# Kernel tuning notes

Hardware: AMD Instinct MI355X
Metric: run time of the kernel (lower is better)

## Reference

```python
import jax, jax.numpy as jnp
import numpy as np

T = 40           # rollout steps
ATT_TEMP = 5.0   # Arbiter attention temperature
ACT_CLIP = 3.5


def setup_inputs() -> dict:
    key = jax.random.key(0)
    ks = jax.random.split(key, 6)
    B, D = 262144, 128
    # states: vel >= 0, dx > 0 (dx is a divisor)
    unscaled_s = jax.random.uniform(ks[0], (B, T, 7), dtype=jnp.float32)
    unscaled_s = unscaled_s.at[:, :, 0].set(unscaled_s[:, :, 0] * 20.0 + 5.0)   # vel
    unscaled_s = unscaled_s.at[:, :, 2].set(unscaled_s[:, :, 2] * 4.0 - 2.0)    # dv (leader)
    unscaled_s = unscaled_s.at[:, :, 3].set(unscaled_s[:, :, 3] * 50.0 + 10.0)  # dx (leader)
    unscaled_s = unscaled_s.at[:, :, 5].set(unscaled_s[:, :, 5] * 4.0 - 2.0)    # dv (merger)
    unscaled_s = unscaled_s.at[:, :, 6].set(unscaled_s[:, :, 6] * 50.0 + 10.0)  # dx (merger)
    # idm params: all strictly positive (sqrt + division)
    p = jax.random.uniform(ks[1], (B, 5), dtype=jnp.float32)
    idm_param = jnp.stack([
        p[:, 0] * 10.0 + 20.0,  # desired_v
        p[:, 1] * 1.0 + 0.5,    # desired_tgap
        p[:, 2] * 3.0 + 1.0,    # min_jamx
        p[:, 3] * 2.0 + 0.5,    # max_act
        p[:, 4] * 2.0 + 0.5,    # min_act
    ], axis=1)
    decoder_output = jax.random.normal(ks[2], (B, D), dtype=jnp.float32)
    W1 = jax.random.normal(ks[3], (D, 100), dtype=jnp.float32) * 0.05
    b1 = jnp.zeros((100,), dtype=jnp.float32)
    W2 = jax.random.normal(ks[4], (100, T), dtype=jnp.float32) * 0.05
    b2 = jnp.zeros((T,), dtype=jnp.float32)
    return {"unscaled_s": unscaled_s, "idm_param": idm_param,
            "decoder_output": decoder_output, "W1": W1, "b1": b1, "W2": W2, "b2": b2}


def _idm_driver(vel, dv, dx, idm_param):
    # vel/dv/dx: [B, T, 1]; idm_param: [B, 5]
    p = idm_param[:, None, :]  # [B, 1, 5]
    desired_v, desired_tgap, min_jamx, max_act, min_act = (
        p[..., 0:1], p[..., 1:2], p[..., 2:3], p[..., 3:4], p[..., 4:5])
    desired_gap = min_jamx + desired_tgap * vel + vel * dv / (2.0 * jnp.sqrt(max_act * min_act))
    act = max_act * (1.0 - (vel / desired_v) ** 4 - (desired_gap / dx) ** 2)
    return jnp.clip(act, -ACT_CLIP, ACT_CLIP)


def reference(unscaled_s, idm_param, decoder_output, W1, b1, W2, b2):
    B = unscaled_s.shape[0]
    # The 40-step loop has no cross-step dependency -> fully vectorized over T.
    s = unscaled_s[:, :T, :]                 # [B, T, 7]
    vel = s[:, :, 0:1]
    fl_seq = _idm_driver(vel, s[:, :, 2:3], s[:, :, 3:4], idm_param)  # [B, T, 1]
    fm_seq = _idm_driver(vel, s[:, :, 5:6], s[:, :, 6:7], idm_param)  # [B, T, 1]
    # Arbiter: two dense layers + temperature sigmoid
    h = decoder_output @ W1 + b1
    logits = h @ W2 + b2                      # [B, T]
    att_scores = jax.nn.sigmoid(ATT_TEMP * logits).reshape(B, T, 1)
    act_seq = att_scores * fl_seq + (1.0 - att_scores) * fm_seq
    return act_seq, att_scores
```

## Files before the change

### kernel.cpp

```cpp
#include <hip/hip_runtime.h>


#define TT 40
#define DD 128
#define ACT_CLIP 3.5f
#define ATT_TEMP 5.0f

typedef short short8 __attribute__((ext_vector_type(8)));
typedef float f32x4 __attribute__((ext_vector_type(4)));

__device__ __forceinline__ unsigned int bf16_rne(float v) {
    unsigned int u = __float_as_uint(v);
    return (u + 0x7FFFu + ((u >> 16) & 1u)) >> 16;
}

__global__ __launch_bounds__(256) void precompute_pack(
    const float* __restrict__ W1, const float* __restrict__ b1,
    const float* __restrict__ W2, const float* __restrict__ b2,
    unsigned int* __restrict__ wpack,
    float* __restrict__ bcp)
{
    int idx = blockIdx.x * 256 + threadIdx.x;
    if (idx < 1536) {
        int l   = idx & 63;
        int rec = idx >> 6;
        int h   = rec & 1;
        int sn  = rec >> 1;
        int n   = sn % 3, s = sn / 3;
        int col = n * 16 + (l & 15);
        int k0  = s * 32 + (l >> 4) * 8;
        unsigned short hv[8];
#pragma unroll
        for (int j = 0; j < 8; ++j) {
            float v = 0.0f;
            if (col < TT) {
                int k = k0 + j;
                for (int m = 0; m < 100; ++m)
                    v = fmaf(W1[k * 100 + m], W2[m * TT + col], v);
            }
            unsigned int hi = bf16_rne(v);
            float hif = __uint_as_float(hi << 16);
            unsigned int lo = bf16_rne(v - hif);
            hv[j] = (unsigned short)(h == 0 ? hi : lo);
        }
        uint4 o;
        o.x = hv[0] | ((unsigned)hv[1] << 16);
        o.y = hv[2] | ((unsigned)hv[3] << 16);
        o.z = hv[4] | ((unsigned)hv[5] << 16);
        o.w = hv[6] | ((unsigned)hv[7] << 16);
        reinterpret_cast<uint4*>(wpack)[idx] = o;
    } else if (idx < 1536 + 48) {
        int t = idx - 1536;
        float v = 0.0f;
        if (t < TT) {
            v = b2[t];
            for (int m = 0; m < 100; ++m)
                v = fmaf(b1[m], W2[m * TT + t], v);
        }
        bcp[t] = v;
    }
}

__global__ __launch_bounds__(256, 4) void matvec_att(
    const float* __restrict__ x,
    const unsigned int* __restrict__ wpack,
    const float* __restrict__ bcp,
    float* __restrict__ attout)
{
    __shared__ unsigned int swp[6144];
    __shared__ float sbc[48];
    __shared__ float satt[64 * TT];

    int tid = threadIdx.x;
    {
        const uint4* src = reinterpret_cast<const uint4*>(wpack);
        uint4* dst = reinterpret_cast<uint4*>(swp);
#pragma unroll
        for (int i = 0; i < 6; ++i) dst[tid + 256 * i] = src[tid + 256 * i];
        if (tid < 48) sbc[tid] = bcp[tid];
    }
    __syncthreads();

    int wave = tid >> 6, lane = tid & 63;
    int l15 = lane & 15, lk = lane >> 4;
    size_t row0 = (size_t)blockIdx.x * 64 + wave * 16 + l15;
    const float* xr = x + row0 * DD;

    float4 xv[8];
#pragma unroll
    for (int s = 0; s < 4; ++s) {
        xv[2 * s]     = *reinterpret_cast<const float4*>(xr + s * 32 + lk * 8);
        xv[2 * s + 1] = *reinterpret_cast<const float4*>(xr + s * 32 + lk * 8 + 4);
    }

    f32x4 acc[3] = {f32x4{0,0,0,0}, f32x4{0,0,0,0}, f32x4{0,0,0,0}};

#pragma unroll
    for (int s = 0; s < 4; ++s) {
        float fs[8] = {xv[2*s].x, xv[2*s].y, xv[2*s].z, xv[2*s].w,
                       xv[2*s+1].x, xv[2*s+1].y, xv[2*s+1].z, xv[2*s+1].w};
        union { unsigned int u[4]; short8 v; } ah, al;
#pragma unroll
        for (int p = 0; p < 4; ++p) {
            unsigned int h0 = bf16_rne(fs[2*p]);
            unsigned int h1 = bf16_rne(fs[2*p+1]);
            float f0 = __uint_as_float(h0 << 16);
            float f1 = __uint_as_float(h1 << 16);
            unsigned int l0 = bf16_rne(fs[2*p] - f0);
            unsigned int l1 = bf16_rne(fs[2*p+1] - f1);
            ah.u[p] = h0 | (h1 << 16);
            al.u[p] = l0 | (l1 << 16);
        }
#pragma unroll
        for (int n = 0; n < 3; ++n) {
            int base = (s * 3 + n) * 512;
            short8 bh = *reinterpret_cast<const short8*>(&swp[base + lane * 4]);
            short8 bl = *reinterpret_cast<const short8*>(&swp[base + 256 + lane * 4]);
            acc[n] = __builtin_amdgcn_mfma_f32_16x16x32_bf16(ah.v, bh, acc[n], 0, 0, 0);
            acc[n] = __builtin_amdgcn_mfma_f32_16x16x32_bf16(al.v, bh, acc[n], 0, 0, 0);
            acc[n] = __builtin_amdgcn_mfma_f32_16x16x32_bf16(ah.v, bl, acc[n], 0, 0, 0);
        }
    }

#pragma unroll
    for (int n = 0; n < 3; ++n) {
        int col = n * 16 + l15;
        if (col < TT) {
            float bias = sbc[col];
#pragma unroll
            for (int r = 0; r < 4; ++r) {
                int rowl = wave * 16 + lk * 4 + r;
                float L = acc[n][r] + bias;
                satt[rowl * TT + col] =
                    __builtin_amdgcn_rcpf(1.0f + __expf(-ATT_TEMP * L));
            }
        }
    }
    __syncthreads();

    float4* dst = reinterpret_cast<float4*>(attout + (size_t)blockIdx.x * 64 * TT);
    const float4* s4 = reinterpret_cast<const float4*>(satt);
    for (int i = tid; i < 640; i += 256) dst[i] = s4[i];
}

__global__ __launch_bounds__(320, 8) void epilogue_k(
    const float* __restrict__ us, const float* __restrict__ prm,
    const float* __restrict__ attg,
    float* __restrict__ act)
{
    unsigned int t0 = blockIdx.x * 320u + threadIdx.x;

    const float4* fv = reinterpret_cast<const float4*>(us) + t0 * 7u;
    float f[28];
#pragma unroll
    for (int q = 0; q < 7; ++q) {
        float4 v = fv[q];
        f[q * 4 + 0] = v.x; f[q * 4 + 1] = v.y;
        f[q * 4 + 2] = v.z; f[q * 4 + 3] = v.w;
    }
    float4 a4 = reinterpret_cast<const float4*>(attg)[t0];
    float av[4] = {a4.x, a4.y, a4.z, a4.w};

    unsigned int row_g = t0 / 10u;
    const float* pr = prm + (size_t)row_g * 5u;
    float desired_v    = pr[0];
    float desired_tgap = pr[1];
    float min_jamx     = pr[2];
    float max_act      = pr[3];
    float min_act      = pr[4];
    float inv_dv = __builtin_amdgcn_rcpf(desired_v);
    float coef   = 0.5f / sqrtf(max_act * min_act);

    float ares[4];
#pragma unroll
    for (int tt = 0; tt < 4; ++tt) {
        float vel = f[tt * 7 + 0];
        float dvl = f[tt * 7 + 2], dxl = f[tt * 7 + 3];
        float dvm = f[tt * 7 + 5], dxm = f[tt * 7 + 6];

        float r  = vel * inv_dv;
        float r2 = r * r;
        float common = 1.0f - r2 * r2;
        float base = fmaf(desired_tgap, vel, min_jamx);
        float gl = fmaf(vel * dvl, coef, base);
        float gm = fmaf(vel * dvm, coef, base);
        float ql = gl * __builtin_amdgcn_rcpf(dxl);
        float qm = gm * __builtin_amdgcn_rcpf(dxm);
        float al = max_act * (common - ql * ql);
        float am = max_act * (common - qm * qm);
        al = fminf(fmaxf(al, -ACT_CLIP), ACT_CLIP);
        am = fminf(fmaxf(am, -ACT_CLIP), ACT_CLIP);
        ares[tt] = fmaf(av[tt], al - am, am);
    }
    reinterpret_cast<float4*>(act)[t0] =
        make_float4(ares[0], ares[1], ares[2], ares[3]);
}

extern "C" void kernel_launch(void* const* d_in, const int* in_sizes, int n_in,
                              void* d_out, int out_size, void* d_ws, size_t ws_size,
                              hipStream_t stream) {
    const float* us  = (const float*)d_in[0];
    const float* prm = (const float*)d_in[1];
    const float* x   = (const float*)d_in[2];
    const float* W1  = (const float*)d_in[3];
    const float* b1  = (const float*)d_in[4];
    const float* W2  = (const float*)d_in[5];
    const float* b2  = (const float*)d_in[6];
    float* out = (float*)d_out;

    int B = in_sizes[1] / 5;

    unsigned int* wpack = (unsigned int*)d_ws;
    float* bcp = (float*)((char*)d_ws + 24576);

    float* attout = out + (size_t)B * TT;

    hipLaunchKernelGGL(precompute_pack, dim3(7), dim3(256), 0, stream,
                       W1, b1, W2, b2, wpack, bcp);
    hipLaunchKernelGGL(matvec_att, dim3(B / 64), dim3(256), 0, stream,
                       x, wpack, bcp, attout);
    hipLaunchKernelGGL(epilogue_k, dim3(B / 32), dim3(320), 0, stream,
                       us, prm, attout, out);
}
```

Before: 137.5 us.

## Fuse attention matvec and IDM epilogue into one kernel

Merges the MFMA attention kernel and the IDM epilogue kernel into a single 320-thread kernel. Attention scores stay in shared memory for the blend instead of being re-read from global memory, and one kernel launch is removed. A fifth wave stages the per-row IDM parameters into shared memory while four waves run the matvec. The packed weights are now read straight from global/L2 per wave rather than staged into LDS, which may add some global load traffic.

```diff
diff --git a/kernel.cpp b/kernel.cpp
--- a/kernel.cpp
+++ b/kernel.cpp
@@ -61,139 +61,143 @@
     }
 }
 
-__global__ __launch_bounds__(256, 4) void matvec_att(
+__global__ __launch_bounds__(320, 4) void fused_k(
     const float* __restrict__ x,
     const unsigned int* __restrict__ wpack,
     const float* __restrict__ bcp,
+    const float* __restrict__ us,
+    const float* __restrict__ prm,
+    float* __restrict__ act,
     float* __restrict__ attout)
 {
-    __shared__ unsigned int swp[6144];
-    __shared__ float sbc[48];
     __shared__ float satt[64 * TT];
+    __shared__ float sprm[64 * 5];
 
     int tid = threadIdx.x;
+    size_t blk = blockIdx.x;
+
+    if (tid < 256) {
+        int wave = tid >> 6, lane = tid & 63;
+        int l15 = lane & 15, lk = lane >> 4;
+        size_t row0 = blk * 64 + wave * 16 + l15;
+        const float* xr = x + row0 * DD;
+
+        float4 xv[8];
+#pragma unroll
+        for (int s = 0; s < 4; ++s) {
+            xv[2 * s]     = *reinterpret_cast<const float4*>(xr + s * 32 + lk * 8);
+            xv[2 * s + 1] = *reinterpret_cast<const float4*>(xr + s * 32 + lk * 8 + 4);
+        }
+
+        f32x4 acc[3] = {f32x4{0,0,0,0}, f32x4{0,0,0,0}, f32x4{0,0,0,0}};
+
+#pragma unroll
+        for (int s = 0; s < 4; ++s) {
+            float fs[8] = {xv[2*s].x, xv[2*s].y, xv[2*s].z, xv[2*s].w,
+                           xv[2*s+1].x, xv[2*s+1].y, xv[2*s+1].z, xv[2*s+1].w};
+            union { unsigned int u[4]; short8 v; } ah, al;
+#pragma unroll
+            for (int p = 0; p < 4; ++p) {
+                unsigned int h0 = bf16_rne(fs[2*p]);
+                unsigned int h1 = bf16_rne(fs[2*p+1]);
+                float f0 = __uint_as_float(h0 << 16);
+                float f1 = __uint_as_float(h1 << 16);
+                unsigned int l0 = bf16_rne(fs[2*p] - f0);
+                unsigned int l1 = bf16_rne(fs[2*p+1] - f1);
+                ah.u[p] = h0 | (h1 << 16);
+                al.u[p] = l0 | (l1 << 16);
+            }
+#pragma unroll
+            for (int n = 0; n < 3; ++n) {
+                int base = (s * 3 + n) * 512;
+                short8 bh = *reinterpret_cast<const short8*>(&wpack[base + lane * 4]);
+                short8 bl = *reinterpret_cast<const short8*>(&wpack[base + 256 + lane * 4]);
+                acc[n] = __builtin_amdgcn_mfma_f32_16x16x32_bf16(ah.v, bh, acc[n], 0, 0, 0);
+                acc[n] = __builtin_amdgcn_mfma_f32_16x16x32_bf16(al.v, bh, acc[n], 0, 0, 0);
+                acc[n] = __builtin_amdgcn_mfma_f32_16x16x32_bf16(ah.v, bl, acc[n], 0, 0, 0);
+            }
+        }
+
+#pragma unroll
+        for (int n = 0; n < 3; ++n) {
+            int col = n * 16 + l15;
+            if (col < TT) {
+                float bias = bcp[col];
+#pragma unroll
+                for (int r = 0; r < 4; ++r) {
+                    int rowl = wave * 16 + lk * 4 + r;
+                    float L = acc[n][r] + bias;
+                    satt[rowl * TT + col] =
+                        __builtin_amdgcn_rcpf(1.0f + __expf(-ATT_TEMP * L));
+                }
+            }
+        }
+    } else {
+        int i = tid - 256;
+        const float4* p4 = reinterpret_cast<const float4*>(prm) + blk * 80;
+        float4* s4 = reinterpret_cast<float4*>(sprm);
+        s4[i] = p4[i];
+        if (i < 16) s4[i + 64] = p4[i + 64];
+    }
+    __syncthreads();
+
     {
-        const uint4* src = reinterpret_cast<const uint4*>(wpack);
-        uint4* dst = reinterpret_cast<uint4*>(swp);
-#pragma unroll
-        for (int i = 0; i < 6; ++i) dst[tid + 256 * i] = src[tid + 256 * i];
-        if (tid < 48) sbc[tid] = bcp[tid];
-    }
-    __syncthreads();
-
-    int wave = tid >> 6, lane = tid & 63;
-    int l15 = lane & 15, lk = lane >> 4;
-    size_t row0 = (size_t)blockIdx.x * 64 + wave * 16 + l15;
-    const float* xr = x + row0 * DD;
-
-    float4 xv[8];
-#pragma unroll
-    for (int s = 0; s < 4; ++s) {
-        xv[2 * s]     = *reinterpret_cast<const float4*>(xr + s * 32 + lk * 8);
-        xv[2 * s + 1] = *reinterpret_cast<const float4*>(xr + s * 32 + lk * 8 + 4);
-    }
-
-    f32x4 acc[3] = {f32x4{0,0,0,0}, f32x4{0,0,0,0}, f32x4{0,0,0,0}};
-
-#pragma unroll
-    for (int s = 0; s < 4; ++s) {
-        float fs[8] = {xv[2*s].x, xv[2*s].y, xv[2*s].z, xv[2*s].w,
-                       xv[2*s+1].x, xv[2*s+1].y, xv[2*s+1].z, xv[2*s+1].w};
-        union { unsigned int u[4]; short8 v; } ah, al;
-#pragma unroll
-        for (int p = 0; p < 4; ++p) {
-            unsigned int h0 = bf16_rne(fs[2*p]);
-            unsigned int h1 = bf16_rne(fs[2*p+1]);
-            float f0 = __uint_as_float(h0 << 16);
-            float f1 = __uint_as_float(h1 << 16);
-            unsigned int l0 = bf16_rne(fs[2*p] - f0);
-            unsigned int l1 = bf16_rne(fs[2*p+1] - f1);
-            ah.u[p] = h0 | (h1 << 16);
-            al.u[p] = l0 | (l1 << 16);
-        }
-#pragma unroll
-        for (int n = 0; n < 3; ++n) {
-            int base = (s * 3 + n) * 512;
-            short8 bh = *reinterpret_cast<const short8*>(&swp[base + lane * 4]);
-            short8 bl = *reinterpret_cast<const short8*>(&swp[base + 256 + lane * 4]);
-            acc[n] = __builtin_amdgcn_mfma_f32_16x16x32_bf16(ah.v, bh, acc[n], 0, 0, 0);
-            acc[n] = __builtin_amdgcn_mfma_f32_16x16x32_bf16(al.v, bh, acc[n], 0, 0, 0);
-            acc[n] = __builtin_amdgcn_mfma_f32_16x16x32_bf16(ah.v, bl, acc[n], 0, 0, 0);
-        }
-    }
-
-#pragma unroll
-    for (int n = 0; n < 3; ++n) {
-        int col = n * 16 + l15;
-        if (col < TT) {
-            float bias = sbc[col];
-#pragma unroll
-            for (int r = 0; r < 4; ++r) {
-                int rowl = wave * 16 + lk * 4 + r;
-                float L = acc[n][r] + bias;
-                satt[rowl * TT + col] =
-                    __builtin_amdgcn_rcpf(1.0f + __expf(-ATT_TEMP * L));
-            }
-        }
-    }
-    __syncthreads();
-
-    float4* dst = reinterpret_cast<float4*>(attout + (size_t)blockIdx.x * 64 * TT);
-    const float4* s4 = reinterpret_cast<const float4*>(satt);
-    for (int i = tid; i < 640; i += 256) dst[i] = s4[i];
-}
-
-__global__ __launch_bounds__(320, 8) void epilogue_k(
-    const float* __restrict__ us, const float* __restrict__ prm,
-    const float* __restrict__ attg,
-    float* __restrict__ act)
-{
-    unsigned int t0 = blockIdx.x * 320u + threadIdx.x;
-
-    const float4* fv = reinterpret_cast<const float4*>(us) + t0 * 7u;
-    float f[28];
-#pragma unroll
-    for (int q = 0; q < 7; ++q) {
-        float4 v = fv[q];
-        f[q * 4 + 0] = v.x; f[q * 4 + 1] = v.y;
-        f[q * 4 + 2] = v.z; f[q * 4 + 3] = v.w;
-    }
-    float4 a4 = reinterpret_cast<const float4*>(attg)[t0];
-    float av[4] = {a4.x, a4.y, a4.z, a4.w};
-
-    unsigned int row_g = t0 / 10u;
-    const float* pr = prm + (size_t)row_g * 5u;
-    float desired_v    = pr[0];
-    float desired_tgap = pr[1];
-    float min_jamx     = pr[2];
-    float max_act      = pr[3];
-    float min_act      = pr[4];
-    float inv_dv = __builtin_amdgcn_rcpf(desired_v);
-    float coef   = 0.5f / sqrtf(max_act * min_act);
-
-    float ares[4];
-#pragma unroll
-    for (int tt = 0; tt < 4; ++tt) {
-        float vel = f[tt * 7 + 0];
-        float dvl = f[tt * 7 + 2], dxl = f[tt * 7 + 3];
-        float dvm = f[tt * 7 + 5], dxm = f[tt * 7 + 6];
-
-        float r  = vel * inv_dv;
-        float r2 = r * r;
-        float common = 1.0f - r2 * r2;
-        float base = fmaf(desired_tgap, vel, min_jamx);
-        float gl = fmaf(vel * dvl, coef, base);
-        float gm = fmaf(vel * dvm, coef, base);
-        float ql = gl * __builtin_amdgcn_rcpf(dxl);
-        float qm = gm * __builtin_amdgcn_rcpf(dxm);
-        float al = max_act * (common - ql * ql);
-        float am = max_act * (common - qm * qm);
-        al = fminf(fmaxf(al, -ACT_CLIP), ACT_CLIP);
-        am = fminf(fmaxf(am, -ACT_CLIP), ACT_CLIP);
-        ares[tt] = fmaf(av[tt], al - am, am);
-    }
-    reinterpret_cast<float4*>(act)[t0] =
-        make_float4(ares[0], ares[1], ares[2], ares[3]);
+        float4* dst = reinterpret_cast<float4*>(attout) + blk * 640;
+        const float4* s4 = reinterpret_cast<const float4*>(satt);
+        dst[tid]       = s4[tid];
+        dst[tid + 320] = s4[tid + 320];
+    }
+
+#pragma unroll
+    for (int it = 0; it < 2; ++it) {
+        unsigned int item = (unsigned)tid + it * 320u;
+        unsigned int row_l = item / 10u;
+
+        const float4* fv = reinterpret_cast<const float4*>(us)
+                           + blk * 4480u + item * 7u;
+        float f[28];
+#pragma unroll
+        for (int q = 0; q < 7; ++q) {
+            float4 v = fv[q];
+            f[q * 4 + 0] = v.x; f[q * 4 + 1] = v.y;
+            f[q * 4 + 2] = v.z; f[q * 4 + 3] = v.w;
+        }
+        float4 a4 = reinterpret_cast<const float4*>(satt)[item];
+        float av[4] = {a4.x, a4.y, a4.z, a4.w};
+
+        const float* pr = &sprm[row_l * 5];
+        float desired_v    = pr[0];
+        float desired_tgap = pr[1];
+        float min_jamx     = pr[2];
+        float max_act      = pr[3];
+        float min_act      = pr[4];
+        float inv_dv = __builtin_amdgcn_rcpf(desired_v);
+        float coef   = 0.5f / sqrtf(max_act * min_act);
+
+        float ares[4];
+#pragma unroll
+        for (int tt = 0; tt < 4; ++tt) {
+            float vel = f[tt * 7 + 0];
+            float dvl = f[tt * 7 + 2], dxl = f[tt * 7 + 3];
+            float dvm = f[tt * 7 + 5], dxm = f[tt * 7 + 6];
+
+            float r  = vel * inv_dv;
+            float r2 = r * r;
+            float common = 1.0f - r2 * r2;
+            float base = fmaf(desired_tgap, vel, min_jamx);
+            float gl = fmaf(vel * dvl, coef, base);
+            float gm = fmaf(vel * dvm, coef, base);
+            float ql = gl * __builtin_amdgcn_rcpf(dxl);
+            float qm = gm * __builtin_amdgcn_rcpf(dxm);
+            float al = max_act * (common - ql * ql);
+            float am = max_act * (common - qm * qm);
+            al = fminf(fmaxf(al, -ACT_CLIP), ACT_CLIP);
+            am = fminf(fmaxf(am, -ACT_CLIP), ACT_CLIP);
+            ares[tt] = fmaf(av[tt], al - am, am);
+        }
+        reinterpret_cast<float4*>(act)[blk * 640u + item] =
+            make_float4(ares[0], ares[1], ares[2], ares[3]);
+    }
 }
 
 extern "C" void kernel_launch(void* const* d_in, const int* in_sizes, int n_in,
@@ -217,8 +221,6 @@
 
     hipLaunchKernelGGL(precompute_pack, dim3(7), dim3(256), 0, stream,
                        W1, b1, W2, b2, wpack, bcp);
-    hipLaunchKernelGGL(matvec_att, dim3(B / 64), dim3(256), 0, stream,
-                       x, wpack, bcp, attout);
-    hipLaunchKernelGGL(epilogue_k, dim3(B / 32), dim3(320), 0, stream,
-                       us, prm, attout, out);
-}
+    hipLaunchKernelGGL(fused_k, dim3(B / 64), dim3(320), 0, stream,
+                       x, wpack, bcp, us, prm, out, attout);
+}
```

New measurement: 148.7 us. 8.1% more time.

## Coalesce epilogue state loads through LDS and truncate bf16 split in matvec

Applied to the files above, without the earlier changes.

The epilogue kernel now loads the unscaled state with consecutive threads reading consecutive float4s, stages the values in padded shared memory, and then has each thread read its own 28 floats back from LDS. Before, each thread read 7 strided float4s directly. This targets uncoalesced global access at the cost of LDS traffic, a barrier, and about 39KB of shared memory per block, which limits occupancy. The matvec's hi/lo bf16 split now uses truncation instead of round-to-nearest-even, which removes ALU work but slightly changes the rounding error of the split. The attention store loop is also manually unrolled.

```diff
diff --git a/kernel.cpp b/kernel.cpp
--- a/kernel.cpp
+++ b/kernel.cpp
@@ -83,7 +83,8 @@
 
     int wave = tid >> 6, lane = tid & 63;
     int l15 = lane & 15, lk = lane >> 4;
-    size_t row0 = (size_t)blockIdx.x * 64 + wave * 16 + l15;
+    size_t blk = blockIdx.x;
+    size_t row0 = blk * 64 + wave * 16 + l15;
     const float* xr = x + row0 * DD;
 
     float4 xv[8];
@@ -102,14 +103,13 @@
         union { unsigned int u[4]; short8 v; } ah, al;
 #pragma unroll
         for (int p = 0; p < 4; ++p) {
-            unsigned int h0 = bf16_rne(fs[2*p]);
-            unsigned int h1 = bf16_rne(fs[2*p+1]);
-            float f0 = __uint_as_float(h0 << 16);
-            float f1 = __uint_as_float(h1 << 16);
-            unsigned int l0 = bf16_rne(fs[2*p] - f0);
-            unsigned int l1 = bf16_rne(fs[2*p+1] - f1);
-            ah.u[p] = h0 | (h1 << 16);
-            al.u[p] = l0 | (l1 << 16);
+            unsigned int u0 = __float_as_uint(fs[2*p]);
+            unsigned int u1 = __float_as_uint(fs[2*p+1]);
+            ah.u[p] = (u0 >> 16) | (u1 & 0xFFFF0000u);
+            float r0 = fs[2*p]   - __uint_as_float(u0 & 0xFFFF0000u);
+            float r1 = fs[2*p+1] - __uint_as_float(u1 & 0xFFFF0000u);
+            al.u[p] = (__float_as_uint(r0) >> 16) |
+                      (__float_as_uint(r1) & 0xFFFF0000u);
         }
 #pragma unroll
         for (int n = 0; n < 3; ++n) {
@@ -138,45 +138,56 @@
     }
     __syncthreads();
 
-    float4* dst = reinterpret_cast<float4*>(attout + (size_t)blockIdx.x * 64 * TT);
+    float4* dst = reinterpret_cast<float4*>(attout + blk * 64 * TT);
     const float4* s4 = reinterpret_cast<const float4*>(satt);
-    for (int i = tid; i < 640; i += 256) dst[i] = s4[i];
-}
-
-__global__ __launch_bounds__(320, 8) void epilogue_k(
+    dst[tid]       = s4[tid];
+    dst[tid + 256] = s4[tid + 256];
+    if (tid < 128) dst[tid + 512] = s4[tid + 512];
+}
+
+__global__ __launch_bounds__(320) void epilogue_k(
     const float* __restrict__ us, const float* __restrict__ prm,
     const float* __restrict__ attg,
     float* __restrict__ act)
 {
-    unsigned int t0 = blockIdx.x * 320u + threadIdx.x;
-
-    const float4* fv = reinterpret_cast<const float4*>(us) + t0 * 7u;
-    float f[28];
-#pragma unroll
-    for (int q = 0; q < 7; ++q) {
-        float4 v = fv[q];
-        f[q * 4 + 0] = v.x; f[q * 4 + 1] = v.y;
-        f[q * 4 + 2] = v.z; f[q * 4 + 3] = v.w;
-    }
-    float4 a4 = reinterpret_cast<const float4*>(attg)[t0];
-    float av[4] = {a4.x, a4.y, a4.z, a4.w};
-
-    unsigned int row_g = t0 / 10u;
+    __shared__ float sus[320 * 31];
+
+    int tid = threadIdx.x;
+    size_t blk = blockIdx.x;
+
+    f32x4 a4 = reinterpret_cast<const f32x4*>(attg)[blk * 320u + tid];
+
+    const f32x4* su = reinterpret_cast<const f32x4*>(us) + blk * 2240u;
+#pragma unroll
+    for (int i = 0; i < 7; ++i) {
+        unsigned f = (unsigned)tid + 320u * i;
+        f32x4 v = su[f];
+        unsigned item = f / 7u;
+        unsigned slot = f - item * 7u;
+        float* w = &sus[item * 31u + slot * 4u];
+        w[0] = v.x; w[1] = v.y; w[2] = v.z; w[3] = v.w;
+    }
+
+    unsigned int row_g = (unsigned)(blk * 320u + tid) / 10u;
     const float* pr = prm + (size_t)row_g * 5u;
     float desired_v    = pr[0];
     float desired_tgap = pr[1];
     float min_jamx     = pr[2];
     float max_act      = pr[3];
     float min_act      = pr[4];
+
+    __syncthreads();
+
     float inv_dv = __builtin_amdgcn_rcpf(desired_v);
     float coef   = 0.5f / sqrtf(max_act * min_act);
 
+    const float* fp = &sus[(unsigned)tid * 31u];
     float ares[4];
 #pragma unroll
     for (int tt = 0; tt < 4; ++tt) {
-        float vel = f[tt * 7 + 0];
-        float dvl = f[tt * 7 + 2], dxl = f[tt * 7 + 3];
-        float dvm = f[tt * 7 + 5], dxm = f[tt * 7 + 6];
+        float vel = fp[tt * 7 + 0];
+        float dvl = fp[tt * 7 + 2], dxl = fp[tt * 7 + 3];
+        float dvm = fp[tt * 7 + 5], dxm = fp[tt * 7 + 6];
 
         float r  = vel * inv_dv;
         float r2 = r * r;
@@ -190,10 +201,11 @@
         float am = max_act * (common - qm * qm);
         al = fminf(fmaxf(al, -ACT_CLIP), ACT_CLIP);
         am = fminf(fmaxf(am, -ACT_CLIP), ACT_CLIP);
-        ares[tt] = fmaf(av[tt], al - am, am);
-    }
-    reinterpret_cast<float4*>(act)[t0] =
-        make_float4(ares[0], ares[1], ares[2], ares[3]);
+        float a = (tt == 0) ? a4.x : (tt == 1) ? a4.y : (tt == 2) ? a4.z : a4.w;
+        ares[tt] = fmaf(a, al - am, am);
+    }
+    f32x4 res = {ares[0], ares[1], ares[2], ares[3]};
+    reinterpret_cast<f32x4*>(act)[blk * 320u + tid] = res;
 }
 
 extern "C" void kernel_launch(void* const* d_in, const int* in_sizes, int n_in,
```

Measured after the change: 131.3 us. 1.05x faster.
